# Optimization experiments

Measured on AMD Instinct MI355X. Metric: run time of the kernel, lower is better.

Reference implementation:

```python
import jax, jax.numpy as jnp
import numpy as np

N, E, P, D = 100000, 800000, 100000, 128

def setup_inputs() -> dict:
    key = jax.random.key(0)
    ks = jax.random.split(key, 24)
    def w(k, i, o):
        return jax.random.normal(k, (i, o), jnp.float32) * (1.0 / np.sqrt(i))
    inp = {
        'x': jax.random.normal(ks[0], (N, D), jnp.float32),
        'src': jax.random.randint(ks[1], (E,), 0, N, jnp.int32),
        'dst': jax.random.randint(ks[2], (E,), 0, N, jnp.int32),
        'pos_src': jax.random.randint(ks[3], (P,), 0, N, jnp.int32),
        'pos_dst': jax.random.randint(ks[4], (P,), 0, N, jnp.int32),
        'neg_src': jax.random.randint(ks[5], (P,), 0, N, jnp.int32),
        'neg_dst': jax.random.randint(ks[6], (P,), 0, N, jnp.int32),
        # SAGEConv params: fc_self, fc_neigh (+bias) per layer
        'Ws0': w(ks[7], D, D), 'Wn0': w(ks[8], D, D), 'b0': jnp.zeros((D,), jnp.float32),
        'Ws1': w(ks[9], D, D), 'Wn1': w(ks[10], D, D), 'b1': jnp.zeros((D,), jnp.float32),
        'Ws2': w(ks[11], D, D), 'Wn2': w(ks[12], D, D), 'b2': jnp.zeros((D,), jnp.float32),
        # predictor MLP: D->D->D->2
        'Wp0': w(ks[13], D, D), 'bp0': jnp.zeros((D,), jnp.float32),
        'Wp1': w(ks[14], D, D), 'bp1': jnp.zeros((D,), jnp.float32),
        'Wp2': w(ks[15], D, 2), 'bp2': jnp.zeros((2,), jnp.float32),
    }
    return inp

def _sage_layer(h, src, dst, n, Ws, Wn, b, act):
    # mean aggregation over in-neighbors (gather -> segment_sum -> divide)
    msum = jax.ops.segment_sum(h[src], dst, num_segments=n)      # [N, D]
    deg = jax.ops.segment_sum(jnp.ones_like(dst, jnp.float32), dst, num_segments=n)
    h_neigh = msum / jnp.maximum(deg, 1.0)[:, None]
    out = h @ Ws + h_neigh @ Wn + b
    return jax.nn.relu(out) if act else out

def _predict(hs, hd, Wp0, bp0, Wp1, bp1, Wp2, bp2):
    z = hs * hd
    z = jax.nn.relu(z @ Wp0 + bp0)
    z = jax.nn.relu(z @ Wp1 + bp1)
    return jax.nn.softmax(z @ Wp2 + bp2, axis=1)[:, 1]

def reference(x, src, dst, pos_src, pos_dst, neg_src, neg_dst,
              Ws0, Wn0, b0, Ws1, Wn1, b1, Ws2, Wn2, b2,
              Wp0, bp0, Wp1, bp1, Wp2, bp2):
    n = x.shape[0]
    h = _sage_layer(x, src, dst, n, Ws0, Wn0, b0, True)
    h = _sage_layer(h, src, dst, n, Ws1, Wn1, b1, True)
    h = _sage_layer(h, src, dst, n, Ws2, Wn2, b2, False)
    pos = _predict(h[pos_src], h[pos_dst], Wp0, bp0, Wp1, bp1, Wp2, bp2)
    neg = _predict(h[neg_src], h[neg_dst], Wp0, bp0, Wp1, bp1, Wp2, bp2)
    return (pos, neg)
```

## Files before the change

### kernel.cpp

```cpp
#include <hip/hip_runtime.h>
#include <cstdint>
#include <cstddef>
#include <cmath>

#define D 128

typedef short bf16x8 __attribute__((ext_vector_type(8)));
typedef float f32x4 __attribute__((ext_vector_type(4)));

__device__ __forceinline__ ushort f2b(float f) {
  uint x = __float_as_uint(f);
  uint r = ((x >> 16) & 1u) + 0x7fffu;
  return (ushort)((x + r) >> 16);
}
__device__ __forceinline__ float b2f(ushort u) {
  return __uint_as_float(((uint)u) << 16);
}

__global__ __launch_bounds__(256) void k_degree_p(const int* __restrict__ dst, int E,
    int* __restrict__ deg, float scale, int CE) {
  int part = blockIdx.x & 7, chunk = blockIdx.x >> 3;
  long base = (long)chunk * CE;
  for (int i = threadIdx.x; i < CE; i += 256) {
    long e = base + i;
    if (e < E) {
      int d = dst[e];
      int p = (int)((float)d * scale); if (p > 7) p = 7;
      if (p == part) atomicAdd(&deg[d], 1);
    }
  }
}

__global__ __launch_bounds__(256) void k_fill_p(const int* __restrict__ src,
    const int* __restrict__ dst, int E, int* __restrict__ cursor,
    int* __restrict__ csrc, float scale, int CE) {
  int part = blockIdx.x & 7, chunk = blockIdx.x >> 3;
  long base = (long)chunk * CE;
  for (int i = threadIdx.x; i < CE; i += 256) {
    long e = base + i;
    if (e < E) {
      int d = dst[e];
      int p = (int)((float)d * scale); if (p > 7) p = 7;
      if (p == part) {
        int s = src[e];
        int pos = atomicAdd(&cursor[d], 1);
        csrc[pos] = s;
      }
    }
  }
}

#define SCAN_T 256
#define SCAN_E 4
#define SCAN_CHUNK (SCAN_T * SCAN_E)

__global__ void k_scan_partial(const int* __restrict__ deg, int n, int* __restrict__ part) {
  __shared__ int s[SCAN_T];
  int base = blockIdx.x * SCAN_CHUNK;
  int sum = 0;
  for (int i = 0; i < SCAN_E; ++i) {
    int idx = base + (int)threadIdx.x * SCAN_E + i;
    if (idx < n) sum += deg[idx];
  }
  s[threadIdx.x] = sum; __syncthreads();
  for (int ofs = SCAN_T / 2; ofs > 0; ofs >>= 1) {
    if ((int)threadIdx.x < ofs) s[threadIdx.x] += s[threadIdx.x + ofs];
    __syncthreads();
  }
  if (threadIdx.x == 0) part[blockIdx.x] = s[0];
}

__global__ void k_scan_part_ex(int* __restrict__ part, int nb) {
  __shared__ int s[1024];
  int v = ((int)threadIdx.x < nb) ? part[threadIdx.x] : 0;
  s[threadIdx.x] = v; __syncthreads();
  for (int ofs = 1; ofs < 1024; ofs <<= 1) {
    int t = ((int)threadIdx.x >= ofs) ? s[threadIdx.x - ofs] : 0;
    __syncthreads();
    s[threadIdx.x] += t;
    __syncthreads();
  }
  if ((int)threadIdx.x < nb) part[threadIdx.x] = s[threadIdx.x] - v;
}

__global__ void k_scan_final(const int* __restrict__ deg, int n, const int* __restrict__ part,
                             int* __restrict__ rowptr, int* __restrict__ cursor, int E) {
  __shared__ int s[SCAN_T];
  int base = blockIdx.x * SCAN_CHUNK;
  int v[SCAN_E]; int local = 0;
  for (int i = 0; i < SCAN_E; ++i) {
    int idx = base + (int)threadIdx.x * SCAN_E + i;
    v[i] = (idx < n) ? deg[idx] : 0;
    local += v[i];
  }
  s[threadIdx.x] = local; __syncthreads();
  for (int ofs = 1; ofs < SCAN_T; ofs <<= 1) {
    int t = ((int)threadIdx.x >= ofs) ? s[threadIdx.x - ofs] : 0;
    __syncthreads();
    s[threadIdx.x] += t;
    __syncthreads();
  }
  int run = part[blockIdx.x] + s[threadIdx.x] - local;
  for (int i = 0; i < SCAN_E; ++i) {
    int idx = base + (int)threadIdx.x * SCAN_E + i;
    if (idx < n) { rowptr[idx] = run; cursor[idx] = run; }
    run += v[i];
  }
  if (blockIdx.x == 0 && threadIdx.x == 0) rowptr[n] = E;
}

__global__ void k_conv_bf16(const float* __restrict__ in, ushort* __restrict__ out, int n8) {
  int i = blockIdx.x * 256 + threadIdx.x;
  if (i >= n8) return;
  float4 a = ((const float4*)in)[i * 2];
  float4 b = ((const float4*)in)[i * 2 + 1];
  ushort4 o0 = {f2b(a.x), f2b(a.y), f2b(a.z), f2b(a.w)};
  ushort4 o1 = {f2b(b.x), f2b(b.y), f2b(b.z), f2b(b.w)};
  ((ushort4*)out)[i * 2] = o0;
  ((ushort4*)out)[i * 2 + 1] = o1;
}

__global__ void k_pack_all(
    const float* __restrict__ Ws0, const float* __restrict__ Wn0,
    const float* __restrict__ Ws1, const float* __restrict__ Wn1,
    const float* __restrict__ Ws2, const float* __restrict__ Wn2,
    const float* __restrict__ Wp0, const float* __restrict__ Wp1,
    ushort* __restrict__ BpL0, ushort* __restrict__ BpL1, ushort* __restrict__ BpL2,
    ushort* __restrict__ BpP0, ushort* __restrict__ BpP1) {
  int o = blockIdx.x * 256 + threadIdx.x;
  const float *W0, *W1; ushort* out; int rel;
  if (o < 32768)       { W0 = Ws0; W1 = Wn0; out = BpL0; rel = o; }
  else if (o < 65536)  { W0 = Ws1; W1 = Wn1; out = BpL1; rel = o - 32768; }
  else if (o < 98304)  { W0 = Ws2; W1 = Wn2; out = BpL2; rel = o - 65536; }
  else if (o < 114688) { W0 = Wp0; W1 = Wp0; out = BpP0; rel = o - 98304; }
  else                 { W0 = Wp1; W1 = Wp1; out = BpP1; rel = o - 114688; }
  int j = rel & 7, lane = (rel >> 3) & 63, t = (rel >> 9) & 7, ks = rel >> 12;
  int k = ks * 32 + ((lane >> 4) * 8) + j;
  int n = t * 16 + (lane & 15);
  const float* W = (k < 128) ? W0 : W1;
  int kk = (k < 128) ? k : k - 128;
  out[rel] = f2b(W[(size_t)kk * D + n]);
}

__global__ __launch_bounds__(256) void k_aggregate2(const ushort* __restrict__ h,
    const int* __restrict__ rowptr, const int* __restrict__ csrc,
    ushort* __restrict__ hn, int N) {
  int tid = threadIdx.x, lane = tid & 63;
  int wid = (int)((blockIdx.x * 256 + tid) >> 6);
  int g = lane >> 4, sub = lane & 15, gb = g << 4;
  int node = wid * 4 + g;
  if (node >= N) return;
  int beg = rowptr[node], end = rowptr[node + 1];
  int dg = end - beg;
  int dd = dg < 16 ? dg : 16;
  int i0 = beg + sub;
  int idxv = (i0 < end) ? csrc[i0] : 0;
  const ushort* hb = h + sub * 8;
  float f[8] = {0.f, 0.f, 0.f, 0.f, 0.f, 0.f, 0.f, 0.f};
  for (int e = 0; e < dd; e += 2) {
    int s0 = __shfl(idxv, gb + e);
    int s1 = __shfl(idxv, gb + e + 1);
    bf16x8 r0 = *(const bf16x8*)(hb + (size_t)s0 * D);
    if (e + 1 < dd) {
      bf16x8 r1 = *(const bf16x8*)(hb + (size_t)s1 * D);
      #pragma unroll
      for (int q = 0; q < 8; ++q)
        f[q] += b2f((ushort)r0[q]) + b2f((ushort)r1[q]);
    } else {
      #pragma unroll
      for (int q = 0; q < 8; ++q) f[q] += b2f((ushort)r0[q]);
    }
  }
  for (int i = beg + 16; i < end; ++i) {
    int s = csrc[i];
    bf16x8 v = *(const bf16x8*)(hb + (size_t)s * D);
    #pragma unroll
    for (int q = 0; q < 8; ++q) f[q] += b2f((ushort)v[q]);
  }
  float inv = (dg > 0) ? (1.0f / (float)dg) : 0.0f;
  bf16x8 o;
  #pragma unroll
  for (int q = 0; q < 8; ++q) o[q] = (short)f2b(f[q] * inv);
  *(bf16x8*)(hn + (size_t)node * D + sub * 8) = o;
}

__global__ __launch_bounds__(256) void k_gemm_mfma(
    const ushort* __restrict__ A, const ushort* __restrict__ An,
    const ushort* __restrict__ Bp, const float* __restrict__ bias,
    ushort* __restrict__ out, int N, int do_relu) {
  int tid = threadIdx.x;
  int wave = tid >> 6, lane = tid & 63;
  int m = lane & 15, kg = lane >> 4;
  int row0 = blockIdx.x * 64 + wave * 16;
  int ar = row0 + m; if (ar >= N) ar = N - 1;
  const ushort* a_self = A  + (size_t)ar * D + kg * 8;
  const ushort* a_nei  = An + (size_t)ar * D + kg * 8;
  f32x4 acc[8];
  #pragma unroll
  for (int t = 0; t < 8; ++t) acc[t] = f32x4{0.f, 0.f, 0.f, 0.f};
  #pragma unroll
  for (int ks = 0; ks < 8; ++ks) {
    const ushort* ap = (ks < 4) ? a_self : a_nei;
    bf16x8 af = *(const bf16x8*)(ap + (ks & 3) * 32);
    const ushort* bb = Bp + (size_t)ks * 4096 + lane * 8;
    #pragma unroll
    for (int t = 0; t < 8; ++t)
      acc[t] = __builtin_amdgcn_mfma_f32_16x16x32_bf16(af, *(const bf16x8*)(bb + t * 512), acc[t], 0, 0, 0);
  }
  #pragma unroll
  for (int t = 0; t < 8; ++t) {
    int c = t * 16 + m;
    float bv = bias[c];
    #pragma unroll
    for (int i = 0; i < 4; ++i) {
      int r = row0 + kg * 4 + i;
      float v = acc[t][i] + bv;
      if (do_relu) v = fmaxf(v, 0.f);
      if (r < N) out[(size_t)r * D + c] = f2b(v);
    }
  }
}

__global__ __launch_bounds__(256) void k_predict_mfma(
    const ushort* __restrict__ h,
    const int* __restrict__ ps, const int* __restrict__ pd,
    const int* __restrict__ ns, const int* __restrict__ nd,
    const ushort* __restrict__ Bp0, const float* __restrict__ bp0,
    const ushort* __restrict__ Bp1, const float* __restrict__ bp1,
    const float* __restrict__ Wp2, const float* __restrict__ bp2,
    float* __restrict__ outp, int P, int pb) {
  __shared__ __align__(16) ushort z1p[4][2048];
  int bi = blockIdx.x;
  const int* sidx; const int* didx; float* op;
  if (bi >= pb) { sidx = ns; didx = nd; op = outp + P; bi -= pb; }
  else          { sidx = ps; didx = pd; op = outp; }
  int tid = threadIdx.x;
  int wave = tid >> 6, lane = tid & 63;
  int m = lane & 15, kg = lane >> 4;
  int pair0 = bi * 64 + wave * 16;
  int prow = pair0 + m; int pr = (prow < P) ? prow : P - 1;
  int si = sidx[pr], di = didx[pr];
  const ushort* hs = h + (size_t)si * D + kg * 8;
  const ushort* hd = h + (size_t)di * D + kg * 8;
  f32x4 acc[8];
  #pragma unroll
  for (int t = 0; t < 8; ++t) acc[t] = f32x4{0.f, 0.f, 0.f, 0.f};
  #pragma unroll
  for (int ks = 0; ks < 4; ++ks) {
    bf16x8 as8 = *(const bf16x8*)(hs + ks * 32);
    bf16x8 ad8 = *(const bf16x8*)(hd + ks * 32);
    bf16x8 af;
    #pragma unroll
    for (int j = 0; j < 8; ++j) {
      float p = b2f((ushort)as8[j]) * b2f((ushort)ad8[j]);
      af[j] = (short)f2b(p);
    }
    const ushort* bb = Bp0 + (size_t)ks * 4096 + lane * 8;
    #pragma unroll
    for (int t = 0; t < 8; ++t)
      acc[t] = __builtin_amdgcn_mfma_f32_16x16x32_bf16(af, *(const bf16x8*)(bb + t * 512), acc[t], 0, 0, 0);
  }
  ushort* zp = &z1p[wave][0];
  #pragma unroll
  for (int t = 0; t < 8; ++t) {
    int c = t * 16 + m;
    float bv = bp0[c];
    int ks2 = c >> 5, kg2 = (c >> 3) & 3, j2 = c & 7;
    #pragma unroll
    for (int i = 0; i < 4; ++i) {
      float v = fmaxf(acc[t][i] + bv, 0.f);
      int l2 = kg2 * 16 + kg * 4 + i;
      zp[(ks2 * 64 + l2) * 8 + j2] = f2b(v);
    }
  }
  __syncthreads();
  #pragma unroll
  for (int t = 0; t < 8; ++t) acc[t] = f32x4{0.f, 0.f, 0.f, 0.f};
  #pragma unroll
  for (int ks = 0; ks < 4; ++ks) {
    bf16x8 af = *(const bf16x8*)(zp + (ks * 64 + lane) * 8);
    const ushort* bb = Bp1 + (size_t)ks * 4096 + lane * 8;
    #pragma unroll
    for (int t = 0; t < 8; ++t)
      acc[t] = __builtin_amdgcn_mfma_f32_16x16x32_bf16(af, *(const bf16x8*)(bb + t * 512), acc[t], 0, 0, 0);
  }
  float p0[4] = {0.f, 0.f, 0.f, 0.f}, p1[4] = {0.f, 0.f, 0.f, 0.f};
  #pragma unroll
  for (int t = 0; t < 8; ++t) {
    int c = t * 16 + m;
    float bv = bp1[c];
    float wa = Wp2[(size_t)c * 2], wb = Wp2[(size_t)c * 2 + 1];
    #pragma unroll
    for (int i = 0; i < 4; ++i) {
      float z = fmaxf(acc[t][i] + bv, 0.f);
      p0[i] += z * wa;
      p1[i] += z * wb;
    }
  }
  #pragma unroll
  for (int msk = 1; msk <= 8; msk <<= 1) {
    #pragma unroll
    for (int i = 0; i < 4; ++i) {
      p0[i] += __shfl_xor(p0[i], msk);
      p1[i] += __shfl_xor(p1[i], msk);
    }
  }
  if (m == 0) {
    float c0 = bp2[0], c1 = bp2[1];
    #pragma unroll
    for (int i = 0; i < 4; ++i) {
      int r = pair0 + kg * 4 + i;
      if (r < P) {
        float l0 = p0[i] + c0, l1 = p1[i] + c1;
        op[r] = 1.0f / (1.0f + expf(l0 - l1));
      }
    }
  }
}

extern "C" void kernel_launch(void* const* d_in, const int* in_sizes, int n_in,
                              void* d_out, int out_size, void* d_ws, size_t ws_size,
                              hipStream_t stream) {
  const float* x       = (const float*)d_in[0];
  const int*   src     = (const int*)d_in[1];
  const int*   dst     = (const int*)d_in[2];
  const int*   pos_src = (const int*)d_in[3];
  const int*   pos_dst = (const int*)d_in[4];
  const int*   neg_src = (const int*)d_in[5];
  const int*   neg_dst = (const int*)d_in[6];
  const float* Ws0 = (const float*)d_in[7],  *Wn0 = (const float*)d_in[8],  *b0 = (const float*)d_in[9];
  const float* Ws1 = (const float*)d_in[10], *Wn1 = (const float*)d_in[11], *b1 = (const float*)d_in[12];
  const float* Ws2 = (const float*)d_in[13], *Wn2 = (const float*)d_in[14], *b2 = (const float*)d_in[15];
  const float* Wp0 = (const float*)d_in[16], *bp0 = (const float*)d_in[17];
  const float* Wp1 = (const float*)d_in[18], *bp1 = (const float*)d_in[19];
  const float* Wp2 = (const float*)d_in[20], *bp2 = (const float*)d_in[21];
  const int N = in_sizes[0] / D;
  const int E = in_sizes[1];
  const int P = in_sizes[3];
  float* outp = (float*)d_out;

  char* ws = (char*)d_ws;
  size_t off = 0;
  auto alloc = [&](size_t bytes) -> void* {
    void* p = ws + off;
    off += (bytes + 255) & ~(size_t)255;
    return p;
  };
  ushort* xb    = (ushort*)alloc((size_t)N * D * 2);
  ushort* h1    = (ushort*)alloc((size_t)N * D * 2);
  ushort* h2    = (ushort*)alloc((size_t)N * D * 2);
  ushort* hn    = (ushort*)alloc((size_t)N * D * 2);
  ushort* BpL0  = (ushort*)alloc(256 * D * 2);
  ushort* BpL1  = (ushort*)alloc(256 * D * 2);
  ushort* BpL2  = (ushort*)alloc(256 * D * 2);
  ushort* BpP0  = (ushort*)alloc(128 * D * 2);
  ushort* BpP1  = (ushort*)alloc(128 * D * 2);
  int*    deg    = (int*)alloc((size_t)N * 4);
  int*    rowptr = (int*)alloc((size_t)(N + 1) * 4);
  int*    cursor = (int*)alloc((size_t)N * 4);
  int*    part   = (int*)alloc(4096);
  int*    csrc   = (int*)alloc((size_t)E * 4);
  (void)ws_size; (void)n_in; (void)out_size;

  const float pscale = 8.0f / (float)N;
  const int CB = 96;
  const int CE = (E + CB - 1) / CB;

  hipMemsetAsync(deg, 0, (size_t)N * 4, stream);
  k_degree_p<<<8 * CB, 256, 0, stream>>>(dst, E, deg, pscale, CE);
  int nb = (N + SCAN_CHUNK - 1) / SCAN_CHUNK;
  k_scan_partial<<<nb, SCAN_T, 0, stream>>>(deg, N, part);
  k_scan_part_ex<<<1, 1024, 0, stream>>>(part, nb);
  k_scan_final<<<nb, SCAN_T, 0, stream>>>(deg, N, part, rowptr, cursor, E);
  k_fill_p<<<8 * CB, 256, 0, stream>>>(src, dst, E, cursor, csrc, pscale, CE);

  int n8 = N * D / 8;
  k_conv_bf16<<<(n8 + 255) / 256, 256, 0, stream>>>(x, xb, n8);
  k_pack_all<<<512, 256, 0, stream>>>(Ws0, Wn0, Ws1, Wn1, Ws2, Wn2, Wp0, Wp1,
                                      BpL0, BpL1, BpL2, BpP0, BpP1);

  int aggb = (N + 15) / 16;
  int gemb = (N + 63) / 64;
  k_aggregate2<<<aggb, 256, 0, stream>>>(xb, rowptr, csrc, hn, N);
  k_gemm_mfma<<<gemb, 256, 0, stream>>>(xb, hn, BpL0, b0, h1, N, 1);
  k_aggregate2<<<aggb, 256, 0, stream>>>(h1, rowptr, csrc, hn, N);
  k_gemm_mfma<<<gemb, 256, 0, stream>>>(h1, hn, BpL1, b1, h2, N, 1);
  k_aggregate2<<<aggb, 256, 0, stream>>>(h2, rowptr, csrc, hn, N);
  k_gemm_mfma<<<gemb, 256, 0, stream>>>(h2, hn, BpL2, b2, xb, N, 0);

  int pb = (P + 63) / 64;
  k_predict_mfma<<<2 * pb, 256, 0, stream>>>(xb, pos_src, pos_dst, neg_src, neg_dst,
                                             BpP0, bp0, BpP1, bp1, Wp2, bp2, outp, P, pb);
}
```

Before: 463.8 us.

## Fuse whole GNN pipeline into one cooperative persistent kernel with grid syncs

Replaces the sequence of separate kernel launches (degree, scan, fill, conversion, packing, three aggregate+GEMM layers, predictor) with a single cooperative persistent kernel. Each phase becomes a grid-stride device function, and phases are separated by grid.sync(). This removes per-launch overhead and the idle gaps between kernels. In exchange, the grid is capped at occupancy×256 blocks, which may cut latency hiding in the gather-heavy aggregate phases, and every grid.sync adds its own cost. A fallback runs the phases as separate kernels if the cooperative launch fails.

```diff
diff --git a/kernel.cpp b/kernel.cpp
--- a/kernel.cpp
+++ b/kernel.cpp
@@ -1,9 +1,13 @@
 #include <hip/hip_runtime.h>
+#include <hip/hip_cooperative_groups.h>
 #include <cstdint>
 #include <cstddef>
 #include <cmath>
 
+namespace cg = cooperative_groups;
+
 #define D 128
+#define NT 256
 
 typedef short bf16x8 __attribute__((ext_vector_type(8)));
 typedef float f32x4 __attribute__((ext_vector_type(4)));
@@ -16,328 +20,403 @@
 __device__ __forceinline__ float b2f(ushort u) {
   return __uint_as_float(((uint)u) << 16);
 }
-
-__global__ __launch_bounds__(256) void k_degree_p(const int* __restrict__ dst, int E,
-    int* __restrict__ deg, float scale, int CE) {
+__device__ __forceinline__ int pis(int l) {
+  return (l & 0x20) | ((l & 3) << 3) | (((l >> 4) & 1) << 2) | ((l >> 2) & 3);
+}
+
+struct MegaP {
+  const float* x;
+  const int* src; const int* dst;
+  const int* ps; const int* pd; const int* ns; const int* nd;
+  const float *Ws0, *Wn0, *b0, *Ws1, *Wn1, *b1, *Ws2, *Wn2, *b2;
+  const float *Wp0, *bp0, *Wp1, *bp1, *Wp2, *bp2;
+  ushort *xb, *h1, *h2, *hn;
+  ushort *BpL0, *BpL1, *BpL2, *BpP0, *BpP1;
+  int *deg, *rowptr, *cursor, *partials, *csrc;
+  float* outp;
+  int N, E, P, CE;
+  float pscale;
+};
+
+__device__ void prep_phase(const MegaP& P) {
+  int TOTg = gridDim.x * NT;
+  int gtid = blockIdx.x * NT + threadIdx.x;
+  for (int i = gtid; i < P.N; i += TOTg) P.deg[i] = 0;
+  int n8 = P.N * (D / 8);
+  const float4* xin = (const float4*)P.x;
+  for (int i = gtid; i < n8; i += TOTg) {
+    float4 a = xin[i * 2], b = xin[i * 2 + 1];
+    ushort4 o0 = {f2b(a.x), f2b(a.y), f2b(a.z), f2b(a.w)};
+    ushort4 o1 = {f2b(b.x), f2b(b.y), f2b(b.z), f2b(b.w)};
+    ((ushort4*)P.xb)[i * 2] = o0;
+    ((ushort4*)P.xb)[i * 2 + 1] = o1;
+  }
+  for (int o = gtid; o < 131072; o += TOTg) {
+    const float *W0, *W1; ushort* outw; int rel;
+    if (o < 32768)       { W0 = P.Ws0; W1 = P.Wn0; outw = P.BpL0; rel = o; }
+    else if (o < 65536)  { W0 = P.Ws1; W1 = P.Wn1; outw = P.BpL1; rel = o - 32768; }
+    else if (o < 98304)  { W0 = P.Ws2; W1 = P.Wn2; outw = P.BpL2; rel = o - 65536; }
+    else if (o < 114688) { W0 = P.Wp0; W1 = P.Wp0; outw = P.BpP0; rel = o - 98304; }
+    else                 { W0 = P.Wp1; W1 = P.Wp1; outw = P.BpP1; rel = o - 114688; }
+    int j = rel & 7, lane = (rel >> 3) & 63, t = (rel >> 9) & 7, ks = rel >> 12;
+    int k = ks * 32 + ((lane >> 4) * 8) + j;
+    int n = t * 16 + (lane & 15);
+    const float* W = (k < 128) ? W0 : W1;
+    int kk = (k < 128) ? k : k - 128;
+    outw[rel] = f2b(W[(size_t)kk * D + n]);
+  }
+}
+
+__device__ void degree_phase(const MegaP& P) {
   int part = blockIdx.x & 7, chunk = blockIdx.x >> 3;
-  long base = (long)chunk * CE;
-  for (int i = threadIdx.x; i < CE; i += 256) {
+  long base = (long)chunk * P.CE;
+  for (int i = threadIdx.x; i < P.CE; i += NT) {
     long e = base + i;
-    if (e < E) {
-      int d = dst[e];
-      int p = (int)((float)d * scale); if (p > 7) p = 7;
-      if (p == part) atomicAdd(&deg[d], 1);
-    }
-  }
-}
-
-__global__ __launch_bounds__(256) void k_fill_p(const int* __restrict__ src,
-    const int* __restrict__ dst, int E, int* __restrict__ cursor,
-    int* __restrict__ csrc, float scale, int CE) {
+    if (e < P.E) {
+      int d = P.dst[e];
+      int pp = (int)((float)d * P.pscale); if (pp > 7) pp = 7;
+      if (pp == part) atomicAdd(&P.deg[d], 1);
+    }
+  }
+}
+
+__device__ void scanA_phase(const MegaP& P, int* sint) {
+  int tid = threadIdx.x;
+  int nchunk = (P.N + 1023) >> 10;
+  for (int c = blockIdx.x; c < nchunk; c += gridDim.x) {
+    int basei = c << 10;
+    int sum = 0;
+    #pragma unroll
+    for (int k = 0; k < 4; ++k) {
+      int idx = basei + tid * 4 + k;
+      if (idx < P.N) sum += P.deg[idx];
+    }
+    sint[tid] = sum; __syncthreads();
+    for (int ofs = 128; ofs > 0; ofs >>= 1) {
+      if (tid < ofs) sint[tid] += sint[tid + ofs];
+      __syncthreads();
+    }
+    if (tid == 0) P.partials[c] = sint[0];
+    __syncthreads();
+  }
+}
+
+__device__ void scanB_phase(const MegaP& P, int* sint) {
+  int tid = threadIdx.x;
+  int nchunk = (P.N + 1023) >> 10;
+  if (blockIdx.x == 0) {
+    int v = (tid < nchunk) ? P.partials[tid] : 0;
+    sint[tid] = v; __syncthreads();
+    for (int ofs = 1; ofs < 256; ofs <<= 1) {
+      int t = (tid >= ofs) ? sint[tid - ofs] : 0;
+      __syncthreads();
+      sint[tid] += t;
+      __syncthreads();
+    }
+    if (tid < nchunk) P.partials[tid] = sint[tid] - v;
+  }
+}
+
+__device__ void scanC_phase(const MegaP& P, int* sint) {
+  int tid = threadIdx.x;
+  int nchunk = (P.N + 1023) >> 10;
+  for (int c = blockIdx.x; c < nchunk; c += gridDim.x) {
+    int basei = c << 10;
+    int v[4]; int local = 0;
+    #pragma unroll
+    for (int k = 0; k < 4; ++k) {
+      int idx = basei + tid * 4 + k;
+      v[k] = (idx < P.N) ? P.deg[idx] : 0;
+      local += v[k];
+    }
+    sint[tid] = local; __syncthreads();
+    for (int ofs = 1; ofs < 256; ofs <<= 1) {
+      int t = (tid >= ofs) ? sint[tid - ofs] : 0;
+      __syncthreads();
+      sint[tid] += t;
+      __syncthreads();
+    }
+    int run = P.partials[c] + sint[tid] - local;
+    #pragma unroll
+    for (int k = 0; k < 4; ++k) {
+      int idx = basei + tid * 4 + k;
+      if (idx < P.N) { P.rowptr[idx] = run; P.cursor[idx] = run; }
+      run += v[k];
+    }
+    __syncthreads();
+  }
+  if (blockIdx.x == 0 && tid == 0) P.rowptr[P.N] = P.E;
+}
+
+__device__ void fill_phase(const MegaP& P) {
   int part = blockIdx.x & 7, chunk = blockIdx.x >> 3;
-  long base = (long)chunk * CE;
-  for (int i = threadIdx.x; i < CE; i += 256) {
+  long base = (long)chunk * P.CE;
+  for (int i = threadIdx.x; i < P.CE; i += NT) {
     long e = base + i;
-    if (e < E) {
-      int d = dst[e];
-      int p = (int)((float)d * scale); if (p > 7) p = 7;
-      if (p == part) {
-        int s = src[e];
-        int pos = atomicAdd(&cursor[d], 1);
-        csrc[pos] = s;
-      }
-    }
-  }
-}
-
-#define SCAN_T 256
-#define SCAN_E 4
-#define SCAN_CHUNK (SCAN_T * SCAN_E)
-
-__global__ void k_scan_partial(const int* __restrict__ deg, int n, int* __restrict__ part) {
-  __shared__ int s[SCAN_T];
-  int base = blockIdx.x * SCAN_CHUNK;
-  int sum = 0;
-  for (int i = 0; i < SCAN_E; ++i) {
-    int idx = base + (int)threadIdx.x * SCAN_E + i;
-    if (idx < n) sum += deg[idx];
-  }
-  s[threadIdx.x] = sum; __syncthreads();
-  for (int ofs = SCAN_T / 2; ofs > 0; ofs >>= 1) {
-    if ((int)threadIdx.x < ofs) s[threadIdx.x] += s[threadIdx.x + ofs];
-    __syncthreads();
-  }
-  if (threadIdx.x == 0) part[blockIdx.x] = s[0];
-}
-
-__global__ void k_scan_part_ex(int* __restrict__ part, int nb) {
-  __shared__ int s[1024];
-  int v = ((int)threadIdx.x < nb) ? part[threadIdx.x] : 0;
-  s[threadIdx.x] = v; __syncthreads();
-  for (int ofs = 1; ofs < 1024; ofs <<= 1) {
-    int t = ((int)threadIdx.x >= ofs) ? s[threadIdx.x - ofs] : 0;
-    __syncthreads();
-    s[threadIdx.x] += t;
-    __syncthreads();
-  }
-  if ((int)threadIdx.x < nb) part[threadIdx.x] = s[threadIdx.x] - v;
-}
-
-__global__ void k_scan_final(const int* __restrict__ deg, int n, const int* __restrict__ part,
-                             int* __restrict__ rowptr, int* __restrict__ cursor, int E) {
-  __shared__ int s[SCAN_T];
-  int base = blockIdx.x * SCAN_CHUNK;
-  int v[SCAN_E]; int local = 0;
-  for (int i = 0; i < SCAN_E; ++i) {
-    int idx = base + (int)threadIdx.x * SCAN_E + i;
-    v[i] = (idx < n) ? deg[idx] : 0;
-    local += v[i];
-  }
-  s[threadIdx.x] = local; __syncthreads();
-  for (int ofs = 1; ofs < SCAN_T; ofs <<= 1) {
-    int t = ((int)threadIdx.x >= ofs) ? s[threadIdx.x - ofs] : 0;
-    __syncthreads();
-    s[threadIdx.x] += t;
-    __syncthreads();
-  }
-  int run = part[blockIdx.x] + s[threadIdx.x] - local;
-  for (int i = 0; i < SCAN_E; ++i) {
-    int idx = base + (int)threadIdx.x * SCAN_E + i;
-    if (idx < n) { rowptr[idx] = run; cursor[idx] = run; }
-    run += v[i];
-  }
-  if (blockIdx.x == 0 && threadIdx.x == 0) rowptr[n] = E;
-}
-
-__global__ void k_conv_bf16(const float* __restrict__ in, ushort* __restrict__ out, int n8) {
-  int i = blockIdx.x * 256 + threadIdx.x;
-  if (i >= n8) return;
-  float4 a = ((const float4*)in)[i * 2];
-  float4 b = ((const float4*)in)[i * 2 + 1];
-  ushort4 o0 = {f2b(a.x), f2b(a.y), f2b(a.z), f2b(a.w)};
-  ushort4 o1 = {f2b(b.x), f2b(b.y), f2b(b.z), f2b(b.w)};
-  ((ushort4*)out)[i * 2] = o0;
-  ((ushort4*)out)[i * 2 + 1] = o1;
-}
-
-__global__ void k_pack_all(
-    const float* __restrict__ Ws0, const float* __restrict__ Wn0,
-    const float* __restrict__ Ws1, const float* __restrict__ Wn1,
-    const float* __restrict__ Ws2, const float* __restrict__ Wn2,
-    const float* __restrict__ Wp0, const float* __restrict__ Wp1,
-    ushort* __restrict__ BpL0, ushort* __restrict__ BpL1, ushort* __restrict__ BpL2,
-    ushort* __restrict__ BpP0, ushort* __restrict__ BpP1) {
-  int o = blockIdx.x * 256 + threadIdx.x;
-  const float *W0, *W1; ushort* out; int rel;
-  if (o < 32768)       { W0 = Ws0; W1 = Wn0; out = BpL0; rel = o; }
-  else if (o < 65536)  { W0 = Ws1; W1 = Wn1; out = BpL1; rel = o - 32768; }
-  else if (o < 98304)  { W0 = Ws2; W1 = Wn2; out = BpL2; rel = o - 65536; }
-  else if (o < 114688) { W0 = Wp0; W1 = Wp0; out = BpP0; rel = o - 98304; }
-  else                 { W0 = Wp1; W1 = Wp1; out = BpP1; rel = o - 114688; }
-  int j = rel & 7, lane = (rel >> 3) & 63, t = (rel >> 9) & 7, ks = rel >> 12;
-  int k = ks * 32 + ((lane >> 4) * 8) + j;
-  int n = t * 16 + (lane & 15);
-  const float* W = (k < 128) ? W0 : W1;
-  int kk = (k < 128) ? k : k - 128;
-  out[rel] = f2b(W[(size_t)kk * D + n]);
-}
-
-__global__ __launch_bounds__(256) void k_aggregate2(const ushort* __restrict__ h,
-    const int* __restrict__ rowptr, const int* __restrict__ csrc,
-    ushort* __restrict__ hn, int N) {
+    if (e < P.E) {
+      int d = P.dst[e];
+      int pp = (int)((float)d * P.pscale); if (pp > 7) pp = 7;
+      if (pp == part) {
+        int s = P.src[e];
+        int pos = atomicAdd(&P.cursor[d], 1);
+        P.csrc[pos] = s;
+      }
+    }
+  }
+}
+
+__device__ void agg_phase(const ushort* __restrict__ h, const int* __restrict__ rowptr,
+    const int* __restrict__ csrc, ushort* __restrict__ hn, int N) {
   int tid = threadIdx.x, lane = tid & 63;
-  int wid = (int)((blockIdx.x * 256 + tid) >> 6);
   int g = lane >> 4, sub = lane & 15, gb = g << 4;
-  int node = wid * 4 + g;
-  if (node >= N) return;
-  int beg = rowptr[node], end = rowptr[node + 1];
-  int dg = end - beg;
-  int dd = dg < 16 ? dg : 16;
-  int i0 = beg + sub;
-  int idxv = (i0 < end) ? csrc[i0] : 0;
+  int w0 = (int)((blockIdx.x * NT + tid) >> 6);
+  int Q = (N + 3) >> 2, W = gridDim.x * 4;
   const ushort* hb = h + sub * 8;
-  float f[8] = {0.f, 0.f, 0.f, 0.f, 0.f, 0.f, 0.f, 0.f};
-  for (int e = 0; e < dd; e += 2) {
-    int s0 = __shfl(idxv, gb + e);
-    int s1 = __shfl(idxv, gb + e + 1);
-    bf16x8 r0 = *(const bf16x8*)(hb + (size_t)s0 * D);
-    if (e + 1 < dd) {
-      bf16x8 r1 = *(const bf16x8*)(hb + (size_t)s1 * D);
-      #pragma unroll
-      for (int q = 0; q < 8; ++q)
-        f[q] += b2f((ushort)r0[q]) + b2f((ushort)r1[q]);
-    } else {
-      #pragma unroll
-      for (int q = 0; q < 8; ++q) f[q] += b2f((ushort)r0[q]);
-    }
-  }
-  for (int i = beg + 16; i < end; ++i) {
-    int s = csrc[i];
-    bf16x8 v = *(const bf16x8*)(hb + (size_t)s * D);
-    #pragma unroll
-    for (int q = 0; q < 8; ++q) f[q] += b2f((ushort)v[q]);
-  }
-  float inv = (dg > 0) ? (1.0f / (float)dg) : 0.0f;
-  bf16x8 o;
-  #pragma unroll
-  for (int q = 0; q < 8; ++q) o[q] = (short)f2b(f[q] * inv);
-  *(bf16x8*)(hn + (size_t)node * D + sub * 8) = o;
-}
-
-__global__ __launch_bounds__(256) void k_gemm_mfma(
-    const ushort* __restrict__ A, const ushort* __restrict__ An,
+  for (int q = w0; q < Q; q += W) {
+    int node = q * 4 + g;
+    int beg = 0, end = 0;
+    if (node < N) { beg = rowptr[node]; end = rowptr[node + 1]; }
+    int dg = end - beg;
+    int dd = dg < 16 ? dg : 16;
+    int i0 = beg + sub;
+    int idxv = (i0 < end) ? csrc[i0] : 0;
+    float f[8] = {0.f, 0.f, 0.f, 0.f, 0.f, 0.f, 0.f, 0.f};
+    for (int e = 0; e < dd; e += 2) {
+      int s0 = __shfl(idxv, gb + e);
+      int s1 = __shfl(idxv, gb + e + 1);
+      bf16x8 r0 = *(const bf16x8*)(hb + (size_t)s0 * D);
+      if (e + 1 < dd) {
+        bf16x8 r1 = *(const bf16x8*)(hb + (size_t)s1 * D);
+        #pragma unroll
+        for (int q2 = 0; q2 < 8; ++q2)
+          f[q2] += b2f((ushort)r0[q2]) + b2f((ushort)r1[q2]);
+      } else {
+        #pragma unroll
+        for (int q2 = 0; q2 < 8; ++q2) f[q2] += b2f((ushort)r0[q2]);
+      }
+    }
+    for (int i = beg + 16; i < end; ++i) {
+      int s = csrc[i];
+      bf16x8 v = *(const bf16x8*)(hb + (size_t)s * D);
+      #pragma unroll
+      for (int q2 = 0; q2 < 8; ++q2) f[q2] += b2f((ushort)v[q2]);
+    }
+    if (node < N) {
+      float inv = (dg > 0) ? (1.0f / (float)dg) : 0.0f;
+      bf16x8 o;
+      #pragma unroll
+      for (int q2 = 0; q2 < 8; ++q2) o[q2] = (short)f2b(f[q2] * inv);
+      *(bf16x8*)(hn + (size_t)node * D + sub * 8) = o;
+    }
+  }
+}
+
+__device__ void gemm_phase(const ushort* __restrict__ A, const ushort* __restrict__ An,
     const ushort* __restrict__ Bp, const float* __restrict__ bias,
     ushort* __restrict__ out, int N, int do_relu) {
-  int tid = threadIdx.x;
-  int wave = tid >> 6, lane = tid & 63;
+  int tid = threadIdx.x, wave = tid >> 6, lane = tid & 63;
   int m = lane & 15, kg = lane >> 4;
-  int row0 = blockIdx.x * 64 + wave * 16;
-  int ar = row0 + m; if (ar >= N) ar = N - 1;
-  const ushort* a_self = A  + (size_t)ar * D + kg * 8;
-  const ushort* a_nei  = An + (size_t)ar * D + kg * 8;
-  f32x4 acc[8];
-  #pragma unroll
-  for (int t = 0; t < 8; ++t) acc[t] = f32x4{0.f, 0.f, 0.f, 0.f};
-  #pragma unroll
-  for (int ks = 0; ks < 8; ++ks) {
-    const ushort* ap = (ks < 4) ? a_self : a_nei;
-    bf16x8 af = *(const bf16x8*)(ap + (ks & 3) * 32);
-    const ushort* bb = Bp + (size_t)ks * 4096 + lane * 8;
-    #pragma unroll
-    for (int t = 0; t < 8; ++t)
-      acc[t] = __builtin_amdgcn_mfma_f32_16x16x32_bf16(af, *(const bf16x8*)(bb + t * 512), acc[t], 0, 0, 0);
-  }
-  #pragma unroll
-  for (int t = 0; t < 8; ++t) {
-    int c = t * 16 + m;
-    float bv = bias[c];
-    #pragma unroll
-    for (int i = 0; i < 4; ++i) {
-      int r = row0 + kg * 4 + i;
-      float v = acc[t][i] + bv;
-      if (do_relu) v = fmaxf(v, 0.f);
-      if (r < N) out[(size_t)r * D + c] = f2b(v);
-    }
-  }
-}
-
-__global__ __launch_bounds__(256) void k_predict_mfma(
-    const ushort* __restrict__ h,
+  int tiles = (N + 63) >> 6;
+  for (int t0 = blockIdx.x; t0 < tiles; t0 += gridDim.x) {
+    int row0 = t0 * 64 + wave * 16;
+    int ar = row0 + m; if (ar >= N) ar = N - 1;
+    const ushort* a_self = A  + (size_t)ar * D + kg * 8;
+    const ushort* a_nei  = An + (size_t)ar * D + kg * 8;
+    f32x4 acc[8];
+    #pragma unroll
+    for (int t = 0; t < 8; ++t) acc[t] = f32x4{0.f, 0.f, 0.f, 0.f};
+    #pragma unroll
+    for (int ks = 0; ks < 8; ++ks) {
+      const ushort* ap = (ks < 4) ? a_self : a_nei;
+      bf16x8 af = *(const bf16x8*)(ap + (ks & 3) * 32);
+      const ushort* bb = Bp + (size_t)ks * 4096 + lane * 8;
+      #pragma unroll
+      for (int t = 0; t < 8; ++t)
+        acc[t] = __builtin_amdgcn_mfma_f32_16x16x32_bf16(af, *(const bf16x8*)(bb + t * 512), acc[t], 0, 0, 0);
+    }
+    #pragma unroll
+    for (int t = 0; t < 8; ++t) {
+      int c = t * 16 + m;
+      float bv = bias[c];
+      #pragma unroll
+      for (int i = 0; i < 4; ++i) {
+        int r = row0 + kg * 4 + i;
+        float v = acc[t][i] + bv;
+        if (do_relu) v = fmaxf(v, 0.f);
+        if (r < N) out[(size_t)r * D + c] = f2b(v);
+      }
+    }
+  }
+}
+
+__device__ void pred_phase(ushort* sb, const ushort* __restrict__ h,
     const int* __restrict__ ps, const int* __restrict__ pd,
     const int* __restrict__ ns, const int* __restrict__ nd,
     const ushort* __restrict__ Bp0, const float* __restrict__ bp0,
     const ushort* __restrict__ Bp1, const float* __restrict__ bp1,
     const float* __restrict__ Wp2, const float* __restrict__ bp2,
-    float* __restrict__ outp, int P, int pb) {
-  __shared__ __align__(16) ushort z1p[4][2048];
-  int bi = blockIdx.x;
-  const int* sidx; const int* didx; float* op;
-  if (bi >= pb) { sidx = ns; didx = nd; op = outp + P; bi -= pb; }
-  else          { sidx = ps; didx = pd; op = outp; }
-  int tid = threadIdx.x;
-  int wave = tid >> 6, lane = tid & 63;
+    float* __restrict__ outp, int P) {
+  int tid = threadIdx.x, wave = tid >> 6, lane = tid & 63;
   int m = lane & 15, kg = lane >> 4;
-  int pair0 = bi * 64 + wave * 16;
-  int prow = pair0 + m; int pr = (prow < P) ? prow : P - 1;
-  int si = sidx[pr], di = didx[pr];
-  const ushort* hs = h + (size_t)si * D + kg * 8;
-  const ushort* hd = h + (size_t)di * D + kg * 8;
-  f32x4 acc[8];
-  #pragma unroll
-  for (int t = 0; t < 8; ++t) acc[t] = f32x4{0.f, 0.f, 0.f, 0.f};
-  #pragma unroll
-  for (int ks = 0; ks < 4; ++ks) {
-    bf16x8 as8 = *(const bf16x8*)(hs + ks * 32);
-    bf16x8 ad8 = *(const bf16x8*)(hd + ks * 32);
-    bf16x8 af;
-    #pragma unroll
-    for (int j = 0; j < 8; ++j) {
-      float p = b2f((ushort)as8[j]) * b2f((ushort)ad8[j]);
-      af[j] = (short)f2b(p);
-    }
-    const ushort* bb = Bp0 + (size_t)ks * 4096 + lane * 8;
-    #pragma unroll
-    for (int t = 0; t < 8; ++t)
-      acc[t] = __builtin_amdgcn_mfma_f32_16x16x32_bf16(af, *(const bf16x8*)(bb + t * 512), acc[t], 0, 0, 0);
-  }
-  ushort* zp = &z1p[wave][0];
-  #pragma unroll
-  for (int t = 0; t < 8; ++t) {
-    int c = t * 16 + m;
-    float bv = bp0[c];
-    int ks2 = c >> 5, kg2 = (c >> 3) & 3, j2 = c & 7;
-    #pragma unroll
-    for (int i = 0; i < 4; ++i) {
-      float v = fmaxf(acc[t][i] + bv, 0.f);
-      int l2 = kg2 * 16 + kg * 4 + i;
-      zp[(ks2 * 64 + l2) * 8 + j2] = f2b(v);
-    }
-  }
-  __syncthreads();
-  #pragma unroll
-  for (int t = 0; t < 8; ++t) acc[t] = f32x4{0.f, 0.f, 0.f, 0.f};
-  #pragma unroll
-  for (int ks = 0; ks < 4; ++ks) {
-    bf16x8 af = *(const bf16x8*)(zp + (ks * 64 + lane) * 8);
-    const ushort* bb = Bp1 + (size_t)ks * 4096 + lane * 8;
-    #pragma unroll
-    for (int t = 0; t < 8; ++t)
-      acc[t] = __builtin_amdgcn_mfma_f32_16x16x32_bf16(af, *(const bf16x8*)(bb + t * 512), acc[t], 0, 0, 0);
-  }
-  float p0[4] = {0.f, 0.f, 0.f, 0.f}, p1[4] = {0.f, 0.f, 0.f, 0.f};
-  #pragma unroll
-  for (int t = 0; t < 8; ++t) {
-    int c = t * 16 + m;
-    float bv = bp1[c];
-    float wa = Wp2[(size_t)c * 2], wb = Wp2[(size_t)c * 2 + 1];
-    #pragma unroll
-    for (int i = 0; i < 4; ++i) {
-      float z = fmaxf(acc[t][i] + bv, 0.f);
-      p0[i] += z * wa;
-      p1[i] += z * wb;
-    }
-  }
-  #pragma unroll
-  for (int msk = 1; msk <= 8; msk <<= 1) {
-    #pragma unroll
-    for (int i = 0; i < 4; ++i) {
-      p0[i] += __shfl_xor(p0[i], msk);
-      p1[i] += __shfl_xor(p1[i], msk);
-    }
-  }
-  if (m == 0) {
-    float c0 = bp2[0], c1 = bp2[1];
-    #pragma unroll
-    for (int i = 0; i < 4; ++i) {
-      int r = pair0 + kg * 4 + i;
-      if (r < P) {
-        float l0 = p0[i] + c0, l1 = p1[i] + c1;
-        op[r] = 1.0f / (1.0f + expf(l0 - l1));
-      }
-    }
-  }
+  int pl = pis(lane);
+  ushort* zp = sb + wave * 2048;
+  int pb = (P + 63) >> 6;
+  int tiles = 2 * pb;
+  for (int bt = blockIdx.x; bt < tiles; bt += gridDim.x) {
+    int bi = bt; const int* sidx; const int* didx; float* op;
+    if (bi >= pb) { sidx = ns; didx = nd; op = outp + P; bi -= pb; }
+    else          { sidx = ps; didx = pd; op = outp; }
+    int pair0 = bi * 64 + wave * 16;
+    int prow = pair0 + m; int pr = (prow < P) ? prow : P - 1;
+    int si = sidx[pr], di = didx[pr];
+    const ushort* hs = h + (size_t)si * D + kg * 8;
+    const ushort* hd = h + (size_t)di * D + kg * 8;
+    f32x4 acc[8];
+    #pragma unroll
+    for (int t = 0; t < 8; ++t) acc[t] = f32x4{0.f, 0.f, 0.f, 0.f};
+    #pragma unroll
+    for (int ks = 0; ks < 4; ++ks) {
+      bf16x8 as8 = *(const bf16x8*)(hs + ks * 32);
+      bf16x8 ad8 = *(const bf16x8*)(hd + ks * 32);
+      bf16x8 af;
+      #pragma unroll
+      for (int j = 0; j < 8; ++j) {
+        float p = b2f((ushort)as8[j]) * b2f((ushort)ad8[j]);
+        af[j] = (short)f2b(p);
+      }
+      const ushort* bb = Bp0 + (size_t)ks * 4096 + lane * 8;
+      #pragma unroll
+      for (int t = 0; t < 8; ++t)
+        acc[t] = __builtin_amdgcn_mfma_f32_16x16x32_bf16(af, *(const bf16x8*)(bb + t * 512), acc[t], 0, 0, 0);
+    }
+    #pragma unroll
+    for (int t = 0; t < 8; ++t) {
+      int c = t * 16 + m;
+      float bv = bp0[c];
+      int ks2 = c >> 5, kg2 = (c >> 3) & 3, j2 = c & 7;
+      #pragma unroll
+      for (int i = 0; i < 4; ++i) {
+        float v = fmaxf(acc[t][i] + bv, 0.f);
+        int l2 = kg2 * 16 + kg * 4 + i;
+        zp[ks2 * 512 + pis(l2) * 8 + j2] = f2b(v);
+      }
+    }
+    __syncthreads();
+    #pragma unroll
+    for (int t = 0; t < 8; ++t) acc[t] = f32x4{0.f, 0.f, 0.f, 0.f};
+    #pragma unroll
+    for (int ks = 0; ks < 4; ++ks) {
+      bf16x8 af = *(const bf16x8*)(zp + ks * 512 + pl * 8);
+      const ushort* bb = Bp1 + (size_t)ks * 4096 + lane * 8;
+      #pragma unroll
+      for (int t = 0; t < 8; ++t)
+        acc[t] = __builtin_amdgcn_mfma_f32_16x16x32_bf16(af, *(const bf16x8*)(bb + t * 512), acc[t], 0, 0, 0);
+    }
+    float p0[4] = {0.f, 0.f, 0.f, 0.f}, p1[4] = {0.f, 0.f, 0.f, 0.f};
+    #pragma unroll
+    for (int t = 0; t < 8; ++t) {
+      int c = t * 16 + m;
+      float bv = bp1[c];
+      float wa = Wp2[(size_t)c * 2], wb = Wp2[(size_t)c * 2 + 1];
+      #pragma unroll
+      for (int i = 0; i < 4; ++i) {
+        float z = fmaxf(acc[t][i] + bv, 0.f);
+        p0[i] += z * wa;
+        p1[i] += z * wb;
+      }
+    }
+    #pragma unroll
+    for (int msk = 1; msk <= 8; msk <<= 1) {
+      #pragma unroll
+      for (int i = 0; i < 4; ++i) {
+        p0[i] += __shfl_xor(p0[i], msk);
+        p1[i] += __shfl_xor(p1[i], msk);
+      }
+    }
+    if (m == 0) {
+      float c0 = bp2[0], c1 = bp2[1];
+      #pragma unroll
+      for (int i = 0; i < 4; ++i) {
+        int r = pair0 + kg * 4 + i;
+        if (r < P) {
+          float l0 = p0[i] + c0, l1 = p1[i] + c1;
+          op[r] = 1.0f / (1.0f + expf(l0 - l1));
+        }
+      }
+    }
+    __syncthreads();
+  }
+}
+
+__global__ __launch_bounds__(NT) void k_mega(MegaP P) {
+  cg::grid_group grid = cg::this_grid();
+  __shared__ __align__(16) ushort sbuf[8192];
+  int* sint = (int*)sbuf;
+  prep_phase(P);                               grid.sync();
+  degree_phase(P);                             grid.sync();
+  scanA_phase(P, sint);                        grid.sync();
+  scanB_phase(P, sint);                        grid.sync();
+  scanC_phase(P, sint);                        grid.sync();
+  fill_phase(P);                               grid.sync();
+  agg_phase(P.xb, P.rowptr, P.csrc, P.hn, P.N);        grid.sync();
+  gemm_phase(P.xb, P.hn, P.BpL0, P.b0, P.h1, P.N, 1);  grid.sync();
+  agg_phase(P.h1, P.rowptr, P.csrc, P.hn, P.N);        grid.sync();
+  gemm_phase(P.h1, P.hn, P.BpL1, P.b1, P.h2, P.N, 1);  grid.sync();
+  agg_phase(P.h2, P.rowptr, P.csrc, P.hn, P.N);        grid.sync();
+  gemm_phase(P.h2, P.hn, P.BpL2, P.b2, P.xb, P.N, 0);  grid.sync();
+  pred_phase(sbuf, P.xb, P.ps, P.pd, P.ns, P.nd,
+             P.BpP0, P.bp0, P.BpP1, P.bp1, P.Wp2, P.bp2, P.outp, P.P);
+}
+
+__global__ __launch_bounds__(NT) void k_prep_w(MegaP P)   { prep_phase(P); }
+__global__ __launch_bounds__(NT) void k_degree_w(MegaP P) { degree_phase(P); }
+__global__ __launch_bounds__(NT) void k_scanA_w(MegaP P) {
+  __shared__ int s[NT]; scanA_phase(P, s);
+}
+__global__ __launch_bounds__(NT) void k_scanB_w(MegaP P) {
+  __shared__ int s[NT]; scanB_phase(P, s);
+}
+__global__ __launch_bounds__(NT) void k_scanC_w(MegaP P) {
+  __shared__ int s[NT]; scanC_phase(P, s);
+}
+__global__ __launch_bounds__(NT) void k_fill_w(MegaP P)   { fill_phase(P); }
+__global__ __launch_bounds__(NT) void k_agg_w(const ushort* h, const int* rowptr,
+    const int* csrc, ushort* hn, int N) { agg_phase(h, rowptr, csrc, hn, N); }
+__global__ __launch_bounds__(NT) void k_gemm_w(const ushort* A, const ushort* An,
+    const ushort* Bp, const float* bias, ushort* out, int N, int do_relu) {
+  gemm_phase(A, An, Bp, bias, out, N, do_relu);
+}
+__global__ __launch_bounds__(NT) void k_pred_w(const ushort* h,
+    const int* ps, const int* pd, const int* ns, const int* nd,
+    const ushort* Bp0, const float* bp0, const ushort* Bp1, const float* bp1,
+    const float* Wp2, const float* bp2, float* outp, int P) {
+  __shared__ __align__(16) ushort sb[8192];
+  pred_phase(sb, h, ps, pd, ns, nd, Bp0, bp0, Bp1, bp1, Wp2, bp2, outp, P);
 }
 
 extern "C" void kernel_launch(void* const* d_in, const int* in_sizes, int n_in,
                               void* d_out, int out_size, void* d_ws, size_t ws_size,
                               hipStream_t stream) {
-  const float* x       = (const float*)d_in[0];
-  const int*   src     = (const int*)d_in[1];
-  const int*   dst     = (const int*)d_in[2];
-  const int*   pos_src = (const int*)d_in[3];
-  const int*   pos_dst = (const int*)d_in[4];
-  const int*   neg_src = (const int*)d_in[5];
-  const int*   neg_dst = (const int*)d_in[6];
-  const float* Ws0 = (const float*)d_in[7],  *Wn0 = (const float*)d_in[8],  *b0 = (const float*)d_in[9];
-  const float* Ws1 = (const float*)d_in[10], *Wn1 = (const float*)d_in[11], *b1 = (const float*)d_in[12];
-  const float* Ws2 = (const float*)d_in[13], *Wn2 = (const float*)d_in[14], *b2 = (const float*)d_in[15];
-  const float* Wp0 = (const float*)d_in[16], *bp0 = (const float*)d_in[17];
-  const float* Wp1 = (const float*)d_in[18], *bp1 = (const float*)d_in[19];
-  const float* Wp2 = (const float*)d_in[20], *bp2 = (const float*)d_in[21];
+  MegaP mp;
+  mp.x   = (const float*)d_in[0];
+  mp.src = (const int*)d_in[1];
+  mp.dst = (const int*)d_in[2];
+  mp.ps  = (const int*)d_in[3];
+  mp.pd  = (const int*)d_in[4];
+  mp.ns  = (const int*)d_in[5];
+  mp.nd  = (const int*)d_in[6];
+  mp.Ws0 = (const float*)d_in[7];  mp.Wn0 = (const float*)d_in[8];  mp.b0 = (const float*)d_in[9];
+  mp.Ws1 = (const float*)d_in[10]; mp.Wn1 = (const float*)d_in[11]; mp.b1 = (const float*)d_in[12];
+  mp.Ws2 = (const float*)d_in[13]; mp.Wn2 = (const float*)d_in[14]; mp.b2 = (const float*)d_in[15];
+  mp.Wp0 = (const float*)d_in[16]; mp.bp0 = (const float*)d_in[17];
+  mp.Wp1 = (const float*)d_in[18]; mp.bp1 = (const float*)d_in[19];
+  mp.Wp2 = (const float*)d_in[20]; mp.bp2 = (const float*)d_in[21];
   const int N = in_sizes[0] / D;
   const int E = in_sizes[1];
   const int P = in_sizes[3];
-  float* outp = (float*)d_out;
+  mp.N = N; mp.E = E; mp.P = P;
+  mp.pscale = 8.0f / (float)N;
+  mp.outp = (float*)d_out;
 
   char* ws = (char*)d_ws;
   size_t off = 0;
@@ -346,49 +425,50 @@
     off += (bytes + 255) & ~(size_t)255;
     return p;
   };
-  ushort* xb    = (ushort*)alloc((size_t)N * D * 2);
-  ushort* h1    = (ushort*)alloc((size_t)N * D * 2);
-  ushort* h2    = (ushort*)alloc((size_t)N * D * 2);
-  ushort* hn    = (ushort*)alloc((size_t)N * D * 2);
-  ushort* BpL0  = (ushort*)alloc(256 * D * 2);
-  ushort* BpL1  = (ushort*)alloc(256 * D * 2);
-  ushort* BpL2  = (ushort*)alloc(256 * D * 2);
-  ushort* BpP0  = (ushort*)alloc(128 * D * 2);
-  ushort* BpP1  = (ushort*)alloc(128 * D * 2);
-  int*    deg    = (int*)alloc((size_t)N * 4);
-  int*    rowptr = (int*)alloc((size_t)(N + 1) * 4);
-  int*    cursor = (int*)alloc((size_t)N * 4);
-  int*    part   = (int*)alloc(4096);
-  int*    csrc   = (int*)alloc((size_t)E * 4);
+  mp.xb   = (ushort*)alloc((size_t)N * D * 2);
+  mp.h1   = (ushort*)alloc((size_t)N * D * 2);
+  mp.h2   = (ushort*)alloc((size_t)N * D * 2);
+  mp.hn   = (ushort*)alloc((size_t)N * D * 2);
+  mp.BpL0 = (ushort*)alloc(256 * D * 2);
+  mp.BpL1 = (ushort*)alloc(256 * D * 2);
+  mp.BpL2 = (ushort*)alloc(256 * D * 2);
+  mp.BpP0 = (ushort*)alloc(128 * D * 2);
+  mp.BpP1 = (ushort*)alloc(128 * D * 2);
+  mp.deg     = (int*)alloc((size_t)N * 4);
+  mp.rowptr  = (int*)alloc((size_t)(N + 1) * 4);
+  mp.cursor  = (int*)alloc((size_t)N * 4);
+  mp.partials= (int*)alloc(1024 * 4);
+  mp.csrc    = (int*)alloc((size_t)E * 4);
   (void)ws_size; (void)n_in; (void)out_size;
 
-  const float pscale = 8.0f / (float)N;
-  const int CB = 96;
-  const int CE = (E + CB - 1) / CB;
-
-  hipMemsetAsync(deg, 0, (size_t)N * 4, stream);
-  k_degree_p<<<8 * CB, 256, 0, stream>>>(dst, E, deg, pscale, CE);
-  int nb = (N + SCAN_CHUNK - 1) / SCAN_CHUNK;
-  k_scan_partial<<<nb, SCAN_T, 0, stream>>>(deg, N, part);
-  k_scan_part_ex<<<1, 1024, 0, stream>>>(part, nb);
-  k_scan_final<<<nb, SCAN_T, 0, stream>>>(deg, N, part, rowptr, cursor, E);
-  k_fill_p<<<8 * CB, 256, 0, stream>>>(src, dst, E, cursor, csrc, pscale, CE);
-
-  int n8 = N * D / 8;
-  k_conv_bf16<<<(n8 + 255) / 256, 256, 0, stream>>>(x, xb, n8);
-  k_pack_all<<<512, 256, 0, stream>>>(Ws0, Wn0, Ws1, Wn1, Ws2, Wn2, Wp0, Wp1,
-                                      BpL0, BpL1, BpL2, BpP0, BpP1);
-
-  int aggb = (N + 15) / 16;
-  int gemb = (N + 63) / 64;
-  k_aggregate2<<<aggb, 256, 0, stream>>>(xb, rowptr, csrc, hn, N);
-  k_gemm_mfma<<<gemb, 256, 0, stream>>>(xb, hn, BpL0, b0, h1, N, 1);
-  k_aggregate2<<<aggb, 256, 0, stream>>>(h1, rowptr, csrc, hn, N);
-  k_gemm_mfma<<<gemb, 256, 0, stream>>>(h1, hn, BpL1, b1, h2, N, 1);
-  k_aggregate2<<<aggb, 256, 0, stream>>>(h2, rowptr, csrc, hn, N);
-  k_gemm_mfma<<<gemb, 256, 0, stream>>>(h2, hn, BpL2, b2, xb, N, 0);
-
-  int pb = (P + 63) / 64;
-  k_predict_mfma<<<2 * pb, 256, 0, stream>>>(xb, pos_src, pos_dst, neg_src, neg_dst,
-                                             BpP0, bp0, BpP1, bp1, Wp2, bp2, outp, P, pb);
-}
+  int occ = 0;
+  hipError_t oe = hipOccupancyMaxActiveBlocksPerMultiprocessor(
+      &occ, (const void*)k_mega, NT, 0);
+  int NBe = ((oe == hipSuccess && occ > 0) ? occ : 1) * 256;
+  if (NBe > 1024) NBe = 1024;
+  mp.CE = (E + (NBe / 8) - 1) / (NBe / 8);
+
+  void* kargs[] = { (void*)&mp };
+  hipError_t le = hipLaunchCooperativeKernel((const void*)k_mega, dim3(NBe),
+                                             dim3(NT), kargs, 0, stream);
+  if (le != hipSuccess) {
+    int aggb = (N + 15) / 16;
+    int gemb = (N + 63) / 64;
+    int pb2  = 2 * ((P + 63) / 64);
+    k_prep_w  <<<NBe, NT, 0, stream>>>(mp);
+    k_degree_w<<<NBe, NT, 0, stream>>>(mp);
+    k_scanA_w <<<256, NT, 0, stream>>>(mp);
+    k_scanB_w <<<1,   NT, 0, stream>>>(mp);
+    k_scanC_w <<<256, NT, 0, stream>>>(mp);
+    k_fill_w  <<<NBe, NT, 0, stream>>>(mp);
+    k_agg_w <<<aggb, NT, 0, stream>>>(mp.xb, mp.rowptr, mp.csrc, mp.hn, N);
+    k_gemm_w<<<gemb, NT, 0, stream>>>(mp.xb, mp.hn, mp.BpL0, mp.b0, mp.h1, N, 1);
+    k_agg_w <<<aggb, NT, 0, stream>>>(mp.h1, mp.rowptr, mp.csrc, mp.hn, N);
+    k_gemm_w<<<gemb, NT, 0, stream>>>(mp.h1, mp.hn, mp.BpL1, mp.b1, mp.h2, N, 1);
+    k_agg_w <<<aggb, NT, 0, stream>>>(mp.h2, mp.rowptr, mp.csrc, mp.hn, N);
+    k_gemm_w<<<gemb, NT, 0, stream>>>(mp.h2, mp.hn, mp.BpL2, mp.b2, mp.xb, N, 0);
+    k_pred_w<<<pb2, NT, 0, stream>>>(mp.xb, mp.ps, mp.pd, mp.ns, mp.nd,
+                                     mp.BpP0, mp.bp0, mp.BpP1, mp.bp1,
+                                     mp.Wp2, mp.bp2, mp.outp, P);
+  }
+}
```

Measured after the change: 1.196 ms. +157.9%, slower.
